# Optimization experiments

Hardware: AMD Instinct MI355X
Metric: run time of the kernel (lower is better)

## Reference

```python
import jax, jax.numpy as jnp
import numpy as np

B, S, D = 4, 2048, 1024
H = 16
HD = D // H  # 64


def setup_inputs() -> dict:
    key = jax.random.key(0)
    ks = jax.random.split(key, 8)
    scale = 1.0 / np.sqrt(D)
    return {
        "hidden_states": jax.random.normal(ks[0], (B, S, D), dtype=jnp.float32),
        "attention_mask": jnp.ones((B, 1, 1, S), dtype=jnp.int32),
        "Wq": jax.random.normal(ks[1], (D, D), dtype=jnp.float32) * scale,
        "bq": jax.random.normal(ks[2], (D,), dtype=jnp.float32) * 0.02,
        "Wk": jax.random.normal(ks[3], (D, D), dtype=jnp.float32) * scale,
        "bk": jax.random.normal(ks[4], (D,), dtype=jnp.float32) * 0.02,
        "Wv": jax.random.normal(ks[5], (D, D), dtype=jnp.float32) * scale,
        "bv": jax.random.normal(ks[6], (D,), dtype=jnp.float32) * 0.02,
    }


def _split_heads(x):
    # [b, t, (h d)] -> [b, h, t, d]
    b, t, _ = x.shape
    return x.reshape(b, t, H, HD).transpose(0, 2, 1, 3)


def reference(hidden_states, attention_mask, Wq, bq, Wk, bk, Wv, bv):
    # Linear projections (torch Linear: x @ W.T + b)
    q = _split_heads(hidden_states @ Wq.T + bq)
    k = _split_heads(hidden_states @ Wk.T + bk)
    v = _split_heads(hidden_states @ Wv.T + bv)

    # scaled dot-product scores: [b, h, s, s]
    scores = jnp.einsum("bhqd,bhkd->bhqk", q, k) / np.sqrt(HD)

    s = scores.shape[-1]
    causal = jnp.tril(jnp.ones((s, s), dtype=bool))[None, None]
    neg_inf = jnp.float32(-jnp.inf)
    scores = jnp.where(causal, scores, neg_inf)
    # attention_mask is 0/1 keep mask: [b, 1, 1, s]
    scores = jnp.where(attention_mask == 0, neg_inf, scores)

    probs = jax.nn.softmax(scores, axis=-1)  # dropout p=0 (eval)
    ctx = jnp.einsum("bhqk,bhkd->bhqd", probs, v)
    # [b, h, t, d] -> [b, t, h*d]
    return ctx.transpose(0, 2, 1, 3).reshape(hidden_states.shape[0], s, D)
```

## Files before the change

### kernel.cpp

```cpp
#include <hip/hip_runtime.h>
#include <hip/hip_bf16.h>
#include <math.h>


#define B_ 4
#define S_ 2048
#define D_ 1024
#define H_ 16
#define HD_ 64
#define M_ (B_ * S_)

typedef unsigned short u16;
typedef unsigned int u32;
typedef __attribute__((ext_vector_type(4))) float f32x4;
typedef __attribute__((ext_vector_type(8))) short bf16x8;

__device__ __forceinline__ u16 f2bfu_rn(float x) {
    u32 u = __builtin_bit_cast(u32, x);
    return (u16)((u + 0x8000u) >> 16);
}

__device__ __forceinline__ void gl2lds16(const void* g, void* l) {
    __builtin_amdgcn_global_load_lds(
        (const __attribute__((address_space(1))) u32*)g,
        (__attribute__((address_space(3))) u32*)l, 16, 0, 0);
}

#define XN  8388608u
#define WN  1048576u
__global__ __launch_bounds__(256) void convert_bf16(
    const float* __restrict__ X,  const float* __restrict__ Wq,
    const float* __restrict__ Wk, const float* __restrict__ Wv,
    u16* __restrict__ Xb, u16* __restrict__ Wqb,
    u16* __restrict__ Wkb, u16* __restrict__ Wvb)
{
    size_t idx = ((size_t)blockIdx.x * 256 + threadIdx.x) * 8;
    const float* src; u16* dst; size_t off;
    if (idx < XN)                { src = X;  dst = Xb;  off = idx; }
    else if (idx < XN + WN)      { src = Wq; dst = Wqb; off = idx - XN; }
    else if (idx < XN + 2 * WN)  { src = Wk; dst = Wkb; off = idx - XN - WN; }
    else                         { src = Wv; dst = Wvb; off = idx - XN - 2 * WN; }
    float4 a = *(const float4*)(src + off);
    float4 b = *(const float4*)(src + off + 4);
    uint4 o;
    o.x = (u32)f2bfu_rn(a.x) | ((u32)f2bfu_rn(a.y) << 16);
    o.y = (u32)f2bfu_rn(a.z) | ((u32)f2bfu_rn(a.w) << 16);
    o.z = (u32)f2bfu_rn(b.x) | ((u32)f2bfu_rn(b.y) << 16);
    o.w = (u32)f2bfu_rn(b.z) | ((u32)f2bfu_rn(b.w) << 16);
    *(uint4*)(dst + off) = o;
}

#define QSCALE 0.18033688011112042f

__global__ __launch_bounds__(256) void qkv_mfma(
    const u16* __restrict__ Xb,
    const u16* __restrict__ Wqb, const u16* __restrict__ Wkb,
    const u16* __restrict__ Wvb,
    const float* __restrict__ bq, const float* __restrict__ bk,
    const float* __restrict__ bv,
    u16* __restrict__ Qb, u16* __restrict__ Kb, u16* __restrict__ Vtb)
{
    const int which = blockIdx.z;
    const u16* Asrc; const u16* Bsrc; const float* bias; u16* Out;
    int m0, n0;
    if (which == 0)      { Asrc = Xb;  Bsrc = Wqb; bias = bq; Out = Qb;
                           m0 = blockIdx.y * 128; n0 = blockIdx.x * 128; }
    else if (which == 1) { Asrc = Xb;  Bsrc = Wkb; bias = bk; Out = Kb;
                           m0 = blockIdx.y * 128; n0 = blockIdx.x * 128; }
    else                 { Asrc = Wvb; Bsrc = Xb;  bias = bv; Out = Vtb;
                           m0 = blockIdx.x * 128; n0 = blockIdx.y * 128; }

    __shared__ u16 As[128][64];
    __shared__ u16 Bs[128][64];

    const int t = threadIdx.x;
    const int wave = t >> 6, lane = t & 63;
    const int qd = lane >> 4, l15 = lane & 15;
    const int wm = wave >> 1, wn = wave & 1;

    const f32x4 zero = {0.f, 0.f, 0.f, 0.f};
    f32x4 acc[4][4];
#pragma unroll
    for (int i = 0; i < 4; ++i)
#pragma unroll
        for (int j = 0; j < 4; ++j) acc[i][j] = zero;

    for (int k0 = 0; k0 < D_; k0 += 64) {
        __syncthreads();
#pragma unroll
        for (int i = 0; i < 4; ++i) {
            int r0  = (wave * 4 + i) * 8;
            int row = r0 + (lane >> 3);
            int g   = (lane & 7) ^ (row & 7);
            gl2lds16(Asrc + (size_t)(m0 + row) * D_ + k0 + g * 8, &As[r0][0]);
            gl2lds16(Bsrc + (size_t)(n0 + row) * D_ + k0 + g * 8, &Bs[r0][0]);
        }
        __syncthreads();
#pragma unroll
        for (int ks = 0; ks < 2; ++ks) {
            bf16x8 af[4], bf[4];
#pragma unroll
            for (int mt = 0; mt < 4; ++mt) {
                int row = wm * 64 + mt * 16 + l15;
                int p = (ks * 4 + qd) ^ (row & 7);
                af[mt] = *(const bf16x8*)&As[row][p * 8];
            }
#pragma unroll
            for (int nt = 0; nt < 4; ++nt) {
                int row = wn * 64 + nt * 16 + l15;
                int p = (ks * 4 + qd) ^ (row & 7);
                bf[nt] = *(const bf16x8*)&Bs[row][p * 8];
            }
#pragma unroll
            for (int mt = 0; mt < 4; ++mt)
#pragma unroll
                for (int nt = 0; nt < 4; ++nt)
                    acc[mt][nt] = __builtin_amdgcn_mfma_f32_16x16x32_bf16(
                        af[mt], bf[nt], acc[mt][nt], 0, 0, 0);
        }
    }

    if (which < 2) {
#pragma unroll
        for (int nt = 0; nt < 4; ++nt) {
            int n = n0 + wn * 64 + nt * 16 + l15;
            float bv_ = bias[n];
            int h = n >> 6, hd = n & 63;
#pragma unroll
            for (int mt = 0; mt < 4; ++mt)
#pragma unroll
                for (int r = 0; r < 4; ++r) {
                    int m = m0 + wm * 64 + mt * 16 + qd * 4 + r;
                    int bb = m >> 11, s = m & 2047;
                    float v = acc[mt][nt][r] + bv_;
                    if (which == 0) v *= QSCALE;
                    Out[(((size_t)(bb * H_ + h)) * S_ + s) * HD_ + hd] = f2bfu_rn(v);
                }
        }
    } else {
#pragma unroll
        for (int mt = 0; mt < 4; ++mt)
#pragma unroll
            for (int r = 0; r < 4; ++r) {
                int f = m0 + wm * 64 + mt * 16 + qd * 4 + r;
                float bv_ = bias[f];
                int h = f >> 6, hd = f & 63;
#pragma unroll
                for (int nt = 0; nt < 4; ++nt) {
                    int tok = n0 + wn * 64 + nt * 16 + l15;
                    int bb = tok >> 11, s = tok & 2047;
                    float v = acc[mt][nt][r] + bv_;
                    Out[(((size_t)(bb * H_ + h)) * HD_ + hd) * S_ + s] = f2bfu_rn(v);
                }
            }
    }
}

__global__ __launch_bounds__(256) void attn_chunk(
    const u16* __restrict__ Qb, const u16* __restrict__ Kb,
    const u16* __restrict__ Vtb, const int* __restrict__ amask,
    float* __restrict__ Oout, float* __restrict__ Opart,
    float* __restrict__ L0, float* __restrict__ L1)
{
    const int x = blockIdx.x;
    const int bh = blockIdx.y;
    const int b = bh >> 4, h = bh & 15;
    int qt, jt0, jt1; bool second;
    if (x < 32) { qt = 31 - x; jt0 = 0;  jt1 = min(qt, 15); second = false; }
    else        { qt = 63 - x; jt0 = 16; jt1 = qt;          second = true;  }
    const int q0 = qt * 64;

    const int t = threadIdx.x;
    const int wave = t >> 6, lane = t & 63;
    const int qd = lane >> 4, l15 = lane & 15;

    __shared__ u16 Ks[64][64];
    __shared__ u16 Vts[64][64];
    __shared__ u16 Ps[64][72];
    __shared__ float mb[64];

    const size_t base = (size_t)bh * S_ * HD_;
    const u16* Qg = Qb + base;
    const u16* Kg = Kb + base;
    const u16* Vg = Vtb + base;
    const int* am = amask + b * S_;

    bf16x8 qf[2];
    {
        const u16* qrow = Qg + (size_t)(q0 + wave * 16 + l15) * HD_;
        qf[0] = *(const bf16x8*)(qrow + qd * 8);
        qf[1] = *(const bf16x8*)(qrow + 32 + qd * 8);
    }
    bf16x8 onesf;
    {
        short v = (l15 == 0) ? (short)0x3F80 : (short)0;
        onesf = (bf16x8){v, v, v, v, v, v, v, v};
    }

    const f32x4 zero = {0.f, 0.f, 0.f, 0.f};
    f32x4 o[5];
#pragma unroll
    for (int i = 0; i < 5; ++i) o[i] = zero;

    for (int jt = jt0; jt <= jt1; ++jt) {
        const int j0 = jt * 64;
        __syncthreads();
#pragma unroll
        for (int i = 0; i < 2; ++i) {
            int r0  = (wave * 2 + i) * 8;
            int row = r0 + (lane >> 3);
            int g   = (lane & 7) ^ (row & 7);
            gl2lds16(Kg + (size_t)(j0 + row) * HD_ + g * 8, &Ks[r0][0]);
            gl2lds16(Vg + (size_t)row * S_ + j0 + g * 8, &Vts[r0][0]);
        }
        if (t < 64) mb[t] = (am[j0 + t] == 0) ? -1e30f : 0.0f;
        __syncthreads();

        f32x4 sacc[4];
#pragma unroll
        for (int nt = 0; nt < 4; ++nt) sacc[nt] = zero;
#pragma unroll
        for (int ks = 0; ks < 2; ++ks) {
#pragma unroll
            for (int nt = 0; nt < 4; ++nt) {
                int brow = nt * 16 + l15;
                int bp = (ks * 4 + qd) ^ (brow & 7);
                bf16x8 bf = *(const bf16x8*)&Ks[brow][bp * 8];
                sacc[nt] = __builtin_amdgcn_mfma_f32_16x16x32_bf16(
                    qf[ks], bf, sacc[nt], 0, 0, 0);
            }
        }

        float bias[4];
#pragma unroll
        for (int nt = 0; nt < 4; ++nt) bias[nt] = mb[nt * 16 + l15];
        const bool diag = (jt == qt);
#pragma unroll
        for (int r = 0; r < 4; ++r) {
            int prow = wave * 16 + qd * 4 + r;
#pragma unroll
            for (int nt = 0; nt < 4; ++nt) {
                int col = nt * 16 + l15;
                float s = sacc[nt][r] + bias[nt];
                if (diag && col > prow) s = -1e30f;
                float p = __builtin_amdgcn_exp2f(s);
                Ps[prow][col] = f2bfu_rn(p);
            }
        }

#pragma unroll
        for (int ks = 0; ks < 2; ++ks) {
            int arow = wave * 16 + l15;
            bf16x8 pf = *(const bf16x8*)&Ps[arow][ks * 32 + qd * 8];
#pragma unroll
            for (int nt = 0; nt < 4; ++nt) {
                int brow = nt * 16 + l15;
                int bp = (ks * 4 + qd) ^ (brow & 7);
                bf16x8 vf = *(const bf16x8*)&Vts[brow][bp * 8];
                o[nt] = __builtin_amdgcn_mfma_f32_16x16x32_bf16(
                    pf, vf, o[nt], 0, 0, 0);
            }
            o[4] = __builtin_amdgcn_mfma_f32_16x16x32_bf16(
                pf, onesf, o[4], 0, 0, 0);
        }
    }

    if (!second) {
        if (qt <= 15) {
#pragma unroll
            for (int r = 0; r < 4; ++r) {
                float l = __shfl(o[4][r], lane & 48);
                float inv = 1.0f / l;
                int q = q0 + wave * 16 + qd * 4 + r;
                float* op = Oout + ((size_t)(b * S_ + q)) * D_ + h * HD_;
#pragma unroll
                for (int nt = 0; nt < 4; ++nt)
                    op[nt * 16 + l15] = o[nt][r] * inv;
            }
        } else {
#pragma unroll
            for (int r = 0; r < 4; ++r) {
                int q = q0 + wave * 16 + qd * 4 + r;
                float* op = Oout + ((size_t)(b * S_ + q)) * D_ + h * HD_;
#pragma unroll
                for (int nt = 0; nt < 4; ++nt)
                    op[nt * 16 + l15] = o[nt][r];
                if (l15 == 0) L0[(size_t)bh * S_ + q] = o[4][r];
            }
        }
    } else {
#pragma unroll
        for (int r = 0; r < 4; ++r) {
            int q = q0 + wave * 16 + qd * 4 + r;
            int sh = q - 1024;
            float* op = Opart + ((size_t)bh * 1024 + sh) * HD_;
#pragma unroll
            for (int nt = 0; nt < 4; ++nt)
                op[nt * 16 + l15] = o[nt][r];
            if (l15 == 0) L1[(size_t)bh * 1024 + sh] = o[4][r];
        }
    }
}

__global__ __launch_bounds__(256) void combine(
    float* __restrict__ out, const float* __restrict__ Opart,
    const float* __restrict__ L0, const float* __restrict__ L1)
{
    size_t i = ((size_t)blockIdx.x * 256 + threadIdx.x) * 4;
    int d  = (int)(i & (D_ - 1));
    int bs = (int)(i >> 10);
    int b  = bs >> 10, sh = bs & 1023;
    int s  = sh + 1024;
    int h  = d >> 6;
    int bh = b * H_ + h;
    float l = L0[(size_t)bh * S_ + s] + L1[(size_t)bh * 1024 + sh];
    float inv = 1.0f / l;
    float* op = out + ((size_t)(b * S_ + s)) * D_ + d;
    const float* pp = Opart + ((size_t)bh * 1024 + sh) * HD_ + (d & 63);
    float4 v = *(float4*)op;
    float4 p = *(const float4*)pp;
    v.x = (v.x + p.x) * inv; v.y = (v.y + p.y) * inv;
    v.z = (v.z + p.z) * inv; v.w = (v.w + p.w) * inv;
    *(float4*)op = v;
}

extern "C" void kernel_launch(void* const* d_in, const int* in_sizes, int n_in,
                              void* d_out, int out_size, void* d_ws, size_t ws_size,
                              hipStream_t stream) {
    (void)in_sizes; (void)n_in; (void)out_size; (void)ws_size;
    const float* X    = (const float*)d_in[0];
    const int*   mask = (const int*)d_in[1];
    const float* Wq   = (const float*)d_in[2];
    const float* bq   = (const float*)d_in[3];
    const float* Wk   = (const float*)d_in[4];
    const float* bk   = (const float*)d_in[5];
    const float* Wv   = (const float*)d_in[6];
    const float* bv   = (const float*)d_in[7];
    float* out = (float*)d_out;

    u16* Xb  = (u16*)d_ws;
    u16* Wqb = Xb  + XN;
    u16* Wkb = Wqb + WN;
    u16* Wvb = Wkb + WN;
    u16* Qb  = Wvb + WN;
    u16* Kb  = Qb  + XN;
    u16* Vtb = Kb  + XN;
    float* Opart = (float*)(Vtb + XN);
    float* L0 = Opart + (size_t)64 * 1024 * 64;
    float* L1 = L0 + (size_t)64 * 2048;

    convert_bf16<<<(XN + 3 * WN) / (256 * 8), 256, 0, stream>>>(
        X, Wq, Wk, Wv, Xb, Wqb, Wkb, Wvb);
    qkv_mfma<<<dim3(D_ / 128, M_ / 128, 3), 256, 0, stream>>>(
        Xb, Wqb, Wkb, Wvb, bq, bk, bv, Qb, Kb, Vtb);
    attn_chunk<<<dim3(48, B_ * H_), 256, 0, stream>>>(
        Qb, Kb, Vtb, mask, out, Opart, L0, L1);
    combine<<<(B_ * 1024 * D_ / 4) / 256, 256, 0, stream>>>(out, Opart, L0, L1);
}
```

Baseline: 264.5 us.

## Use 128-row query tiles with double-buffered K/V staging in attention

The attention kernel now handles 128 query rows per block instead of 64, with each wave computing two 16-row M tiles. This lets every K/V LDS fragment be reused twice and halves the grid to 24 blocks per head. K/V tiles are double-buffered so the next tile loads while the current one is computed, which removes one barrier per iteration. MFMA sections are wrapped in s_setprio, and the block-to-work mapping is rebalanced for the causal split. The cost is fewer blocks, which means less parallelism and coarser load balance, plus more registers and LDS per block.

```diff
diff --git a/kernel.cpp b/kernel.cpp
--- a/kernel.cpp
+++ b/kernel.cpp
@@ -165,19 +165,28 @@
     const int x = blockIdx.x;
     const int bh = blockIdx.y;
     const int b = bh >> 4, h = bh & 15;
-    int qt, jt0, jt1; bool second;
-    if (x < 32) { qt = 31 - x; jt0 = 0;  jt1 = min(qt, 15); second = false; }
-    else        { qt = 63 - x; jt0 = 16; jt1 = qt;          second = true;  }
-    const int q0 = qt * 64;
+
+    int qi; bool second;
+    if (x < 9)       { qi = 15 - x; second = false; }
+    else if (x == 9) { qi = 15;     second = true;  }
+    else {
+        int p = x - 10, pi = p >> 1;
+        second = (p & 1) != 0;
+        qi = second ? (14 - pi) : (6 - pi);
+    }
+    const int q0    = qi * 128;
+    const int jtmax = 2 * qi + 1;
+    const int jt0   = second ? 16 : 0;
+    const int jt1   = second ? jtmax : min(jtmax, 15);
 
     const int t = threadIdx.x;
     const int wave = t >> 6, lane = t & 63;
     const int qd = lane >> 4, l15 = lane & 15;
 
-    __shared__ u16 Ks[64][64];
-    __shared__ u16 Vts[64][64];
-    __shared__ u16 Ps[64][72];
-    __shared__ float mb[64];
+    __shared__ u16 Ks[2][64][64];
+    __shared__ u16 Vts[2][64][64];
+    __shared__ u16 Ps[128][72];
+    __shared__ float mb[2][64];
 
     const size_t base = (size_t)bh * S_ * HD_;
     const u16* Qg = Qb + base;
@@ -185,11 +194,12 @@
     const u16* Vg = Vtb + base;
     const int* am = amask + b * S_;
 
-    bf16x8 qf[2];
-    {
-        const u16* qrow = Qg + (size_t)(q0 + wave * 16 + l15) * HD_;
-        qf[0] = *(const bf16x8*)(qrow + qd * 8);
-        qf[1] = *(const bf16x8*)(qrow + 32 + qd * 8);
+    bf16x8 qf[2][2];
+#pragma unroll
+    for (int mt = 0; mt < 2; ++mt) {
+        const u16* qrow = Qg + (size_t)(q0 + wave * 32 + mt * 16 + l15) * HD_;
+        qf[mt][0] = *(const bf16x8*)(qrow + qd * 8);
+        qf[mt][1] = *(const bf16x8*)(qrow + 32 + qd * 8);
     }
     bf16x8 onesf;
     {
@@ -198,107 +208,140 @@
     }
 
     const f32x4 zero = {0.f, 0.f, 0.f, 0.f};
-    f32x4 o[5];
-#pragma unroll
-    for (int i = 0; i < 5; ++i) o[i] = zero;
-
-    for (int jt = jt0; jt <= jt1; ++jt) {
+    f32x4 o[2][5];
+#pragma unroll
+    for (int mt = 0; mt < 2; ++mt)
+#pragma unroll
+        for (int i = 0; i < 5; ++i) o[mt][i] = zero;
+
+    auto STAGE = [&](int jt, int buf) {
         const int j0 = jt * 64;
-        __syncthreads();
 #pragma unroll
         for (int i = 0; i < 2; ++i) {
             int r0  = (wave * 2 + i) * 8;
             int row = r0 + (lane >> 3);
             int g   = (lane & 7) ^ (row & 7);
-            gl2lds16(Kg + (size_t)(j0 + row) * HD_ + g * 8, &Ks[r0][0]);
-            gl2lds16(Vg + (size_t)row * S_ + j0 + g * 8, &Vts[r0][0]);
-        }
-        if (t < 64) mb[t] = (am[j0 + t] == 0) ? -1e30f : 0.0f;
-        __syncthreads();
-
-        f32x4 sacc[4];
-#pragma unroll
-        for (int nt = 0; nt < 4; ++nt) sacc[nt] = zero;
+            gl2lds16(Kg + (size_t)(j0 + row) * HD_ + g * 8, &Ks[buf][r0][0]);
+            gl2lds16(Vg + (size_t)row * S_ + j0 + g * 8, &Vts[buf][r0][0]);
+        }
+        if (t < 64) mb[buf][t] = (am[j0 + t] == 0) ? -1e30f : 0.0f;
+    };
+
+    STAGE(jt0, 0);
+    __syncthreads();
+
+    for (int jt = jt0; jt <= jt1; ++jt) {
+        const int cb = (jt - jt0) & 1;
+        if (jt < jt1) STAGE(jt + 1, cb ^ 1);
+
+        f32x4 sacc[2][4];
+#pragma unroll
+        for (int mt = 0; mt < 2; ++mt)
+#pragma unroll
+            for (int nt = 0; nt < 4; ++nt) sacc[mt][nt] = zero;
+        __builtin_amdgcn_s_setprio(1);
 #pragma unroll
         for (int ks = 0; ks < 2; ++ks) {
 #pragma unroll
             for (int nt = 0; nt < 4; ++nt) {
                 int brow = nt * 16 + l15;
                 int bp = (ks * 4 + qd) ^ (brow & 7);
-                bf16x8 bf = *(const bf16x8*)&Ks[brow][bp * 8];
-                sacc[nt] = __builtin_amdgcn_mfma_f32_16x16x32_bf16(
-                    qf[ks], bf, sacc[nt], 0, 0, 0);
-            }
-        }
+                bf16x8 bfr = *(const bf16x8*)&Ks[cb][brow][bp * 8];
+#pragma unroll
+                for (int mt = 0; mt < 2; ++mt)
+                    sacc[mt][nt] = __builtin_amdgcn_mfma_f32_16x16x32_bf16(
+                        qf[mt][ks], bfr, sacc[mt][nt], 0, 0, 0);
+            }
+        }
+        __builtin_amdgcn_s_setprio(0);
 
         float bias[4];
 #pragma unroll
-        for (int nt = 0; nt < 4; ++nt) bias[nt] = mb[nt * 16 + l15];
-        const bool diag = (jt == qt);
-#pragma unroll
-        for (int r = 0; r < 4; ++r) {
-            int prow = wave * 16 + qd * 4 + r;
-#pragma unroll
-            for (int nt = 0; nt < 4; ++nt) {
-                int col = nt * 16 + l15;
-                float s = sacc[nt][r] + bias[nt];
-                if (diag && col > prow) s = -1e30f;
-                float p = __builtin_amdgcn_exp2f(s);
-                Ps[prow][col] = f2bfu_rn(p);
-            }
-        }
-
+        for (int nt = 0; nt < 4; ++nt) bias[nt] = mb[cb][nt * 16 + l15];
+        const bool nearDiag = (jt >= 2 * qi);
+        const int dq = q0 - jt * 64;
+#pragma unroll
+        for (int mt = 0; mt < 2; ++mt)
+#pragma unroll
+            for (int r = 0; r < 4; ++r) {
+                int prow = wave * 32 + mt * 16 + qd * 4 + r;
+#pragma unroll
+                for (int nt = 0; nt < 4; ++nt) {
+                    int col = nt * 16 + l15;
+                    float s = sacc[mt][nt][r] + bias[nt];
+                    if (nearDiag && col > prow + dq) s = -1e30f;
+                    float p = __builtin_amdgcn_exp2f(s);
+                    Ps[prow][col] = f2bfu_rn(p);
+                }
+            }
+
+        __builtin_amdgcn_s_setprio(1);
 #pragma unroll
         for (int ks = 0; ks < 2; ++ks) {
-            int arow = wave * 16 + l15;
-            bf16x8 pf = *(const bf16x8*)&Ps[arow][ks * 32 + qd * 8];
+            bf16x8 pf[2];
+#pragma unroll
+            for (int mt = 0; mt < 2; ++mt)
+                pf[mt] = *(const bf16x8*)&Ps[wave * 32 + mt * 16 + l15][ks * 32 + qd * 8];
 #pragma unroll
             for (int nt = 0; nt < 4; ++nt) {
                 int brow = nt * 16 + l15;
                 int bp = (ks * 4 + qd) ^ (brow & 7);
-                bf16x8 vf = *(const bf16x8*)&Vts[brow][bp * 8];
-                o[nt] = __builtin_amdgcn_mfma_f32_16x16x32_bf16(
-                    pf, vf, o[nt], 0, 0, 0);
-            }
-            o[4] = __builtin_amdgcn_mfma_f32_16x16x32_bf16(
-                pf, onesf, o[4], 0, 0, 0);
-        }
+                bf16x8 vf = *(const bf16x8*)&Vts[cb][brow][bp * 8];
+#pragma unroll
+                for (int mt = 0; mt < 2; ++mt)
+                    o[mt][nt] = __builtin_amdgcn_mfma_f32_16x16x32_bf16(
+                        pf[mt], vf, o[mt][nt], 0, 0, 0);
+            }
+#pragma unroll
+            for (int mt = 0; mt < 2; ++mt)
+                o[mt][4] = __builtin_amdgcn_mfma_f32_16x16x32_bf16(
+                    pf[mt], onesf, o[mt][4], 0, 0, 0);
+        }
+        __builtin_amdgcn_s_setprio(0);
+
+        if (jt < jt1) __syncthreads();
     }
 
     if (!second) {
-        if (qt <= 15) {
+        if (qi <= 7) {
+#pragma unroll
+            for (int mt = 0; mt < 2; ++mt)
+#pragma unroll
+                for (int r = 0; r < 4; ++r) {
+                    float l = __shfl(o[mt][4][r], lane & 48);
+                    float inv = 1.0f / l;
+                    int q = q0 + wave * 32 + mt * 16 + qd * 4 + r;
+                    float* op = Oout + ((size_t)(b * S_ + q)) * D_ + h * HD_;
+#pragma unroll
+                    for (int nt = 0; nt < 4; ++nt)
+                        op[nt * 16 + l15] = o[mt][nt][r] * inv;
+                }
+        } else {
+#pragma unroll
+            for (int mt = 0; mt < 2; ++mt)
+#pragma unroll
+                for (int r = 0; r < 4; ++r) {
+                    int q = q0 + wave * 32 + mt * 16 + qd * 4 + r;
+                    float* op = Oout + ((size_t)(b * S_ + q)) * D_ + h * HD_;
+#pragma unroll
+                    for (int nt = 0; nt < 4; ++nt)
+                        op[nt * 16 + l15] = o[mt][nt][r];
+                    if (l15 == 0) L0[(size_t)bh * S_ + q] = o[mt][4][r];
+                }
+        }
+    } else {
+#pragma unroll
+        for (int mt = 0; mt < 2; ++mt)
 #pragma unroll
             for (int r = 0; r < 4; ++r) {
-                float l = __shfl(o[4][r], lane & 48);
-                float inv = 1.0f / l;
-                int q = q0 + wave * 16 + qd * 4 + r;
-                float* op = Oout + ((size_t)(b * S_ + q)) * D_ + h * HD_;
+                int q = q0 + wave * 32 + mt * 16 + qd * 4 + r;
+                int sh = q - 1024;
+                float* op = Opart + ((size_t)bh * 1024 + sh) * HD_;
 #pragma unroll
                 for (int nt = 0; nt < 4; ++nt)
-                    op[nt * 16 + l15] = o[nt][r] * inv;
-            }
-        } else {
-#pragma unroll
-            for (int r = 0; r < 4; ++r) {
-                int q = q0 + wave * 16 + qd * 4 + r;
-                float* op = Oout + ((size_t)(b * S_ + q)) * D_ + h * HD_;
-#pragma unroll
-                for (int nt = 0; nt < 4; ++nt)
-                    op[nt * 16 + l15] = o[nt][r];
-                if (l15 == 0) L0[(size_t)bh * S_ + q] = o[4][r];
-            }
-        }
-    } else {
-#pragma unroll
-        for (int r = 0; r < 4; ++r) {
-            int q = q0 + wave * 16 + qd * 4 + r;
-            int sh = q - 1024;
-            float* op = Opart + ((size_t)bh * 1024 + sh) * HD_;
-#pragma unroll
-            for (int nt = 0; nt < 4; ++nt)
-                op[nt * 16 + l15] = o[nt][r];
-            if (l15 == 0) L1[(size_t)bh * 1024 + sh] = o[4][r];
-        }
+                    op[nt * 16 + l15] = o[mt][nt][r];
+                if (l15 == 0) L1[(size_t)bh * 1024 + sh] = o[mt][4][r];
+            }
     }
 }
 
@@ -353,7 +396,7 @@
         X, Wq, Wk, Wv, Xb, Wqb, Wkb, Wvb);
     qkv_mfma<<<dim3(D_ / 128, M_ / 128, 3), 256, 0, stream>>>(
         Xb, Wqb, Wkb, Wvb, bq, bk, bv, Qb, Kb, Vtb);
-    attn_chunk<<<dim3(48, B_ * H_), 256, 0, stream>>>(
+    attn_chunk<<<dim3(24, B_ * H_), 256, 0, stream>>>(
         Qb, Kb, Vtb, mask, out, Opart, L0, L1);
     combine<<<(B_ * 1024 * D_ / 4) / 256, 256, 0, stream>>>(out, Opart, L0, L1);
 }
```

Result: no change. 265.5 us (+0.4%).

## Rewrite QKV GEMM with 8-wave 128x256 tiles and triple-buffered LDS pipeline

Applied to the files above, without the earlier changes.

The QKV projection GEMM now uses 512-thread blocks on 128x256 tiles. LDS is triple-buffered, with async global-to-LDS loads issued two k-steps ahead and interleaved with the MFMA phases, using explicit vmcnt/lgkmcnt waits, barriers and setprio. Block indices are swizzled for better L2 locality. The aim is to hide memory latency and raise MFMA utilisation, at the cost of more LDS per block and fragile hand-tuned synchronisation.

```diff
diff --git a/kernel.cpp b/kernel.cpp
--- a/kernel.cpp
+++ b/kernel.cpp
@@ -52,7 +52,7 @@
 
 #define QSCALE 0.18033688011112042f
 
-__global__ __launch_bounds__(256) void qkv_mfma(
+__global__ __launch_bounds__(512) void qkv_mfma8(
     const u16* __restrict__ Xb,
     const u16* __restrict__ Wqb, const u16* __restrict__ Wkb,
     const u16* __restrict__ Wvb,
@@ -60,23 +60,40 @@
     const float* __restrict__ bv,
     u16* __restrict__ Qb, u16* __restrict__ Kb, u16* __restrict__ Vtb)
 {
-    const int which = blockIdx.z;
+    const int which = blockIdx.y;
+    const int bxl = ((blockIdx.x & 7) << 5) | (blockIdx.x >> 3);
+
     const u16* Asrc; const u16* Bsrc; const float* bias; u16* Out;
     int m0, n0;
     if (which == 0)      { Asrc = Xb;  Bsrc = Wqb; bias = bq; Out = Qb;
-                           m0 = blockIdx.y * 128; n0 = blockIdx.x * 128; }
+                           m0 = (bxl >> 2) * 128; n0 = (bxl & 3) * 256; }
     else if (which == 1) { Asrc = Xb;  Bsrc = Wkb; bias = bk; Out = Kb;
-                           m0 = blockIdx.y * 128; n0 = blockIdx.x * 128; }
+                           m0 = (bxl >> 2) * 128; n0 = (bxl & 3) * 256; }
     else                 { Asrc = Wvb; Bsrc = Xb;  bias = bv; Out = Vtb;
-                           m0 = blockIdx.x * 128; n0 = blockIdx.y * 128; }
-
-    __shared__ u16 As[128][64];
-    __shared__ u16 Bs[128][64];
+                           m0 = (bxl >> 5) * 128; n0 = (bxl & 31) * 256; }
+
+    __shared__ u16 As[3][128][64];
+    __shared__ u16 Bs[3][256][64];
 
     const int t = threadIdx.x;
     const int wave = t >> 6, lane = t & 63;
     const int qd = lane >> 4, l15 = lane & 15;
-    const int wm = wave >> 1, wn = wave & 1;
+    const int wm = wave >> 2, wn = wave & 3;
+
+    auto STAGE_A = [&](int tt, int u) {
+        const int buf = tt % 3, k0 = tt * 64;
+        const int rb = u * 64 + wave * 8;
+        const int r  = rb + (lane >> 3);
+        const int g  = (lane & 7) ^ (r & 7);
+        gl2lds16(Asrc + (size_t)(m0 + r) * D_ + k0 + g * 8, &As[buf][rb][0]);
+    };
+    auto STAGE_B = [&](int tt, int q) {
+        const int buf = tt % 3, k0 = tt * 64;
+        const int rb = q * 64 + wave * 8;
+        const int r  = rb + (lane >> 3);
+        const int g  = (lane & 7) ^ (r & 7);
+        gl2lds16(Bsrc + (size_t)(n0 + r) * D_ + k0 + g * 8, &Bs[buf][rb][0]);
+    };
 
     const f32x4 zero = {0.f, 0.f, 0.f, 0.f};
     f32x4 acc[4][4];
@@ -85,38 +102,79 @@
 #pragma unroll
         for (int j = 0; j < 4; ++j) acc[i][j] = zero;
 
-    for (int k0 = 0; k0 < D_; k0 += 64) {
-        __syncthreads();
-#pragma unroll
-        for (int i = 0; i < 4; ++i) {
-            int r0  = (wave * 4 + i) * 8;
-            int row = r0 + (lane >> 3);
-            int g   = (lane & 7) ^ (row & 7);
-            gl2lds16(Asrc + (size_t)(m0 + row) * D_ + k0 + g * 8, &As[r0][0]);
-            gl2lds16(Bsrc + (size_t)(n0 + row) * D_ + k0 + g * 8, &Bs[r0][0]);
-        }
-        __syncthreads();
-#pragma unroll
-        for (int ks = 0; ks < 2; ++ks) {
-            bf16x8 af[4], bf[4];
-#pragma unroll
-            for (int mt = 0; mt < 4; ++mt) {
-                int row = wm * 64 + mt * 16 + l15;
-                int p = (ks * 4 + qd) ^ (row & 7);
-                af[mt] = *(const bf16x8*)&As[row][p * 8];
-            }
-#pragma unroll
-            for (int nt = 0; nt < 4; ++nt) {
-                int row = wn * 64 + nt * 16 + l15;
-                int p = (ks * 4 + qd) ^ (row & 7);
-                bf[nt] = *(const bf16x8*)&Bs[row][p * 8];
-            }
-#pragma unroll
-            for (int mt = 0; mt < 4; ++mt)
+#pragma unroll
+    for (int u = 0; u < 2; ++u) STAGE_A(0, u);
+#pragma unroll
+    for (int q = 0; q < 4; ++q) STAGE_B(0, q);
+#pragma unroll
+    for (int u = 0; u < 2; ++u) STAGE_A(1, u);
+#pragma unroll
+    for (int q = 0; q < 4; ++q) STAGE_B(1, q);
+    asm volatile("s_waitcnt vmcnt(6)" ::: "memory");
+    __builtin_amdgcn_s_barrier();
+
+    for (int tt = 0; tt < 16; ++tt) {
+        const int buf = tt % 3;
+        const bool st = tt < 14;
+        const int t2 = tt + 2;
+
+        bf16x8 bfv[4][2];
+        bf16x8 af[2];
+
+#pragma unroll
+        for (int nt = 0; nt < 4; ++nt) {
+            const int row = wn * 64 + nt * 16 + l15;
+#pragma unroll
+            for (int ks = 0; ks < 2; ++ks)
+                bfv[nt][ks] = *(const bf16x8*)&Bs[buf][row][((ks * 4 + qd) ^ (row & 7)) * 8];
+        }
+        {
+            const int row = wm * 64 + l15;
+#pragma unroll
+            for (int ks = 0; ks < 2; ++ks)
+                af[ks] = *(const bf16x8*)&As[buf][row][((ks * 4 + qd) ^ (row & 7)) * 8];
+        }
+        if (st) { STAGE_A(t2, 0); STAGE_A(t2, 1); }
+        __builtin_amdgcn_s_barrier();
+        asm volatile("s_waitcnt lgkmcnt(0)" ::: "memory");
+        __builtin_amdgcn_sched_barrier(0);
+        __builtin_amdgcn_s_setprio(1);
+#pragma unroll
+        for (int ks = 0; ks < 2; ++ks)
+#pragma unroll
+            for (int nt = 0; nt < 4; ++nt)
+                acc[0][nt] = __builtin_amdgcn_mfma_f32_16x16x32_bf16(
+                    af[ks], bfv[nt][ks], acc[0][nt], 0, 0, 0);
+        __builtin_amdgcn_s_setprio(0);
+        __builtin_amdgcn_s_barrier();
+
+#pragma unroll
+        for (int mt = 1; mt < 4; ++mt) {
+            const int row = wm * 64 + mt * 16 + l15;
+#pragma unroll
+            for (int ks = 0; ks < 2; ++ks)
+                af[ks] = *(const bf16x8*)&As[buf][row][((ks * 4 + qd) ^ (row & 7)) * 8];
+            if (st) {
+                if (mt == 1)      { STAGE_B(t2, 0); STAGE_B(t2, 1); }
+                else if (mt == 2) { STAGE_B(t2, 2); }
+                else              { STAGE_B(t2, 3); }
+            }
+            __builtin_amdgcn_s_barrier();
+            asm volatile("s_waitcnt lgkmcnt(0)" ::: "memory");
+            __builtin_amdgcn_sched_barrier(0);
+            __builtin_amdgcn_s_setprio(1);
+#pragma unroll
+            for (int ks = 0; ks < 2; ++ks)
 #pragma unroll
                 for (int nt = 0; nt < 4; ++nt)
                     acc[mt][nt] = __builtin_amdgcn_mfma_f32_16x16x32_bf16(
-                        af[mt], bf[nt], acc[mt][nt], 0, 0, 0);
+                        af[ks], bfv[nt][ks], acc[mt][nt], 0, 0, 0);
+            __builtin_amdgcn_s_setprio(0);
+            if (mt == 3) {
+                if (st) asm volatile("s_waitcnt vmcnt(6)" ::: "memory");
+                else    asm volatile("s_waitcnt vmcnt(0)" ::: "memory");
+            }
+            __builtin_amdgcn_s_barrier();
         }
     }
 
@@ -351,7 +409,7 @@
 
     convert_bf16<<<(XN + 3 * WN) / (256 * 8), 256, 0, stream>>>(
         X, Wq, Wk, Wv, Xb, Wqb, Wkb, Wvb);
-    qkv_mfma<<<dim3(D_ / 128, M_ / 128, 3), 256, 0, stream>>>(
+    qkv_mfma8<<<dim3(256, 3), 512, 0, stream>>>(
         Xb, Wqb, Wkb, Wvb, bq, bk, bv, Qb, Kb, Vtb);
     attn_chunk<<<dim3(48, B_ * H_), 256, 0, stream>>>(
         Qb, Kb, Vtb, mask, out, Opart, L0, L1);
```

New measurement: 263.4 us. About the same (-0.4%).
